# Optimization experiments

Measured on AMD Instinct MI355X. Metric: run time of the kernel, lower is better.

## Reference

```python
import jax, jax.numpy as jnp
import numpy as np

N_VERTICES = 2000
N_SENSORY = 784
N_EDGES = 500_000
BATCH = 32
T_STEPS = 5
LR_VALUES = 0.1


def setup_inputs() -> dict:
    key = jax.random.key(0)
    k1, k2, k3 = jax.random.split(key, 3)
    values = jax.random.normal(k1, (BATCH, N_VERTICES), dtype=jnp.float32)
    # weight_init 'normal 0.0' -> std = max(0.01, 0) = 0.01 in the torch module
    weights = jax.random.normal(k2, (N_EDGES,), dtype=jnp.float32) * 0.01
    edge_index = jax.random.randint(k3, (2, N_EDGES), 0, N_VERTICES, dtype=jnp.int32)
    # sensory nodes (first 784) are clamped; only internal nodes update
    update_mask = jnp.arange(N_VERTICES) >= N_SENSORY  # bool [N]
    return {
        "values": values,
        "weights": weights,
        "edge_index": edge_index,
        "update_mask": update_mask,
        "T": T_STEPS,
    }


def reference(values, weights, edge_index, update_mask, T):
    """Iterative predictive-coding message passing.

    Each step:
      pred_i  = sum_{e: dst(e)=i} w_e * f(values[src(e)])   (gather-mul-scatter)
      err     = values - pred
      back_j  = sum_{e: src(e)=j} w_e * err[dst(e)]          (reverse scatter)
      dv      = err - f'(values) * back                      (dE/dx)
      values  = values - lr * dv   (sensory nodes clamped)
    """
    src, dst = edge_index[0], edge_index[1]
    n = values.shape[1]
    mask = update_mask[None, :]

    def step(v, _):
        fx = jnp.tanh(v)                                   # [B, N]
        msg = weights[None, :] * fx[:, src]                # [B, E]
        pred = jax.ops.segment_sum(msg.T, dst, num_segments=n).T  # [B, N]
        err = v - pred                                     # [B, N]
        w_err = weights[None, :] * err[:, dst]             # [B, E]
        back = jax.ops.segment_sum(w_err.T, src, num_segments=n).T  # [B, N]
        fprime = 1.0 - fx * fx                             # tanh'
        dv = err - fprime * back
        v_new = jnp.where(mask, v - LR_VALUES * dv, v)
        return v_new, None

    v_final, _ = jax.lax.scan(step, values, None, length=T)
    return v_final
```

## Files before the change

### kernel.cpp

```cpp
#include <hip/hip_runtime.h>
#include <hip/hip_bf16.h>


#define N_V     2000
#define N_SENS  784
#define N_INT   (N_V - N_SENS)
#define N_E     500000
#define T_STEPS 5
#define LR_VAL  0.1f
#define NVB     (N_V * 32)
#define NVH     (N_V * 16)
#define KP      2016
#define NCH     63
#define NT1     125
#define NT2     76
#define FRAG_N  (2 * NCH * 64 * 8)
#define NBLK    250
#define EPB     2000

typedef float  f32x4 __attribute__((ext_vector_type(4)));
typedef short  s16x8 __attribute__((ext_vector_type(8)));

__device__ __forceinline__ float bits_to_f32(unsigned u) {
    union { unsigned u; float f; } c; c.u = u; return c.f;
}
__device__ __forceinline__ unsigned f32_to_bits(float f) {
    union { float f; unsigned u; } c; c.f = f; return c.u;
}
__device__ __forceinline__ unsigned short f32_to_bf16(float f) {
    unsigned u = f32_to_bits(f);
    return (unsigned short)((u + 0x7FFFu + ((u >> 16) & 1u)) >> 16);
}
__device__ __forceinline__ float bf16_to_f32(unsigned short s) {
    return bits_to_f32((unsigned)s << 16);
}

__device__ __forceinline__ int aposKB(int k, int b) {
    int c = k >> 5, q = (k >> 3) & 3, j = k & 7;
    int h = b >> 4, m = b & 15;
    return (((h * NCH + c) * 64) + q * 16 + m) * 8 + j;
}


__global__ __launch_bounds__(256) void k_cnt(const int* __restrict__ dst,
                                             int* __restrict__ cnt_g,
                                             unsigned short* __restrict__ fxA,
                                             unsigned short* __restrict__ errA) {
    __shared__ int cnt[NT1];
    int b = blockIdx.x;
    {
        int t = b * 256 + threadIdx.x;
        if (t < 16 * 32) {
            int k = 2000 + (t >> 5), bb = t & 31;
            fxA[aposKB(k, bb)] = 0;
            errA[aposKB(k, bb)] = 0;
        }
    }
    for (int i = threadIdx.x; i < NT1; i += 256) cnt[i] = 0;
    __syncthreads();
    int base = b * EPB;
    for (int e = base + threadIdx.x; e < base + EPB; e += 256)
        atomicAdd(&cnt[dst[e] >> 4], 1);
    __syncthreads();
    for (int t = threadIdx.x; t < NT1; t += 256)
        cnt_g[t * 256 + b] = cnt[t];
}

__global__ __launch_bounds__(256) void k_scan_a(const int* __restrict__ cnt_g,
                                                int* __restrict__ base_g,
                                                int* __restrict__ totals) {
    __shared__ int sh[256];
    int t = blockIdx.x, tid = threadIdx.x;
    int v = (tid < NBLK) ? cnt_g[t * 256 + tid] : 0;
    sh[tid] = v;
    __syncthreads();
    for (int off = 1; off < 256; off <<= 1) {
        int x = (tid >= off) ? sh[tid - off] : 0;
        __syncthreads();
        sh[tid] += x;
        __syncthreads();
    }
    if (tid < NBLK) base_g[t * 256 + tid] = sh[tid] - v;
    if (tid == 255) totals[t] = sh[255];
}

__global__ void k_scan_b(const int* __restrict__ totals, int* __restrict__ tile_start) {
    if (threadIdx.x == 0 && blockIdx.x == 0) {
        int acc = 0;
        for (int t = 0; t < NT1; ++t) { tile_start[t] = acc; acc += totals[t]; }
        tile_start[NT1] = acc;
    }
}

__global__ __launch_bounds__(256) void k_place(
        const int* __restrict__ src, const int* __restrict__ dst,
        const float* __restrict__ w, const int* __restrict__ base_g,
        const int* __restrict__ tile_start, unsigned* __restrict__ pk_g) {
    __shared__ int cur[NT1];
    int b = blockIdx.x;
    for (int t = threadIdx.x; t < NT1; t += 256)
        cur[t] = tile_start[t] + base_g[t * 256 + b];
    __syncthreads();
    int base = b * EPB;
    for (int e = base + threadIdx.x; e < base + EPB; e += 256) {
        int d = dst[e];
        unsigned pk = ((unsigned)f32_to_bf16(w[e]) << 16)
                    | ((unsigned)(d & 15) << 11) | (unsigned)src[e];
        int p = atomicAdd(&cur[d >> 4], 1);
        pk_g[p] = pk;
    }
}

__global__ __launch_bounds__(256) void k_build(
        const unsigned* __restrict__ pk_g, const int* __restrict__ tile_start,
        uint4* __restrict__ WAbf4, unsigned short* __restrict__ WAd) {
    __shared__ float acc[8][KP];
    int tile = blockIdx.x >> 1, half = blockIdx.x & 1;
    for (int i = threadIdx.x; i < 8 * KP / 4; i += 256)
        ((float4*)&acc[0][0])[i] = make_float4(0.f, 0.f, 0.f, 0.f);
    __syncthreads();
    int beg = tile_start[tile], end = tile_start[tile + 1];
    for (int e = beg + threadIdx.x; e < end; e += 256) {
        unsigned pk = pk_g[e];
        int row = (int)((pk >> 11) & 15u);
        if ((row >> 3) == half)
            atomicAdd(&acc[row & 7][pk & 0x7FFu], bf16_to_f32((unsigned short)(pk >> 16)));
    }
    __syncthreads();
    for (int i = threadIdx.x; i < 8 * 252; i += 256) {
        int rr = i / 252, g = i - rr * 252;
        int c = g >> 2, q = g & 3;
        int col = g * 8;
        unsigned short r[8];
        #pragma unroll
        for (int j = 0; j < 8; ++j) r[j] = f32_to_bf16(acc[rr][col + j]);
        uint4 val = *(const uint4*)r;
        int m = half * 8 + rr;
        WAbf4[((tile * NCH + c) * 64) + q * 16 + m] = val;
        *(uint4*)(WAd + (size_t)(tile * 16 + m) * KP + col) = val;
    }
}

__global__ void k_trB(const unsigned short* __restrict__ WAd, uint4* __restrict__ WBf4) {
    int t = blockIdx.x * blockDim.x + threadIdx.x;
    if (t < NT2 * NCH * 64) {
        int tile = t / (NCH * 64);
        int rem = t - tile * (NCH * 64);
        int c = rem >> 6, l = rem & 63;
        int jcol = N_SENS + tile * 16 + (l & 15);
        int k0 = c * 32 + (l >> 4) * 8;
        unsigned short r[8];
        #pragma unroll
        for (int j = 0; j < 8; ++j)
            r[j] = (k0 + j < N_V) ? WAd[(size_t)(k0 + j) * KP + jcol] : (unsigned short)0;
        WBf4[t] = *(const uint4*)r;
    }
}

__global__ void k_init(const float* __restrict__ vin, float* __restrict__ v,
                       unsigned short* __restrict__ fxA, float* __restrict__ out) {
    int t = blockIdx.x * blockDim.x + threadIdx.x;
    if (t < NVB) {
        float x = vin[t];
        int b = t / N_V;
        int i = t - b * N_V;
        v[(i << 5) + b] = x;
        fxA[aposKB(i, b)] = f32_to_bf16(tanhf(x));
        if (i < N_SENS) out[t] = x;
    }
}

__global__ __launch_bounds__(256) void k_gemm1(
        const uint4* __restrict__ WAbf4, const uint4* __restrict__ fxA4,
        const float* __restrict__ v_cur, unsigned short* __restrict__ errA) {
    __shared__ float red[1300];
    int bx = blockIdx.x, tid = threadIdx.x;
    int w = tid >> 6, l = tid & 63;
    int tile = bx >> 1, h = bx & 1;
    int cbeg = w * 16;
    const uint4* bp = WAbf4 + (size_t)tile * NCH * 64 + cbeg * 64 + l;
    const uint4* ap = fxA4 + (size_t)h * NCH * 64 + cbeg * 64 + l;
    f32x4 acc = {0.f, 0.f, 0.f, 0.f};
    #pragma unroll
    for (int cc = 0; cc < 16; ++cc) {
        if (cbeg + cc < NCH) {
            uint4 bfrag = bp[cc * 64];
            uint4 a = ap[cc * 64];
            acc = __builtin_amdgcn_mfma_f32_16x16x32_bf16(
                      *(s16x8*)&a, *(s16x8*)&bfrag, acc, 0, 0, 0);
        }
    }
    float* my = &red[w * 325 + l * 5];
    #pragma unroll
    for (int r = 0; r < 4; ++r) my[r] = acc[r];
    __syncthreads();
    if (w == 0) {
        float s[4];
        #pragma unroll
        for (int r = 0; r < 4; ++r)
            s[r] = red[l * 5 + r] + red[325 + l * 5 + r]
                 + red[650 + l * 5 + r] + red[975 + l * 5 + r];
        int i = tile * 16 + (l & 15);
        int q = l >> 4;
        int c2 = i >> 5, q2 = (i >> 3) & 3, j2 = i & 7;
        const float4 v4 = *(const float4*)(v_cur + (i << 5) + h * 16 + q * 4);
        int base = ((h * NCH + c2) * 64 + q2 * 16) * 8 + j2;
        errA[base + (q * 4 + 0) * 8] = f32_to_bf16(v4.x - s[0]);
        errA[base + (q * 4 + 1) * 8] = f32_to_bf16(v4.y - s[1]);
        errA[base + (q * 4 + 2) * 8] = f32_to_bf16(v4.z - s[2]);
        errA[base + (q * 4 + 3) * 8] = f32_to_bf16(v4.w - s[3]);
    }
}

__global__ __launch_bounds__(256) void k_gemm2(
        const uint4* __restrict__ WBf4, const uint4* __restrict__ errA4,
        unsigned short* __restrict__ errA, unsigned short* __restrict__ fxA,
        float* __restrict__ v_cur, float* __restrict__ out, int final_step) {
    __shared__ float red[1300];
    int bx = blockIdx.x, tid = threadIdx.x;
    int w = tid >> 6, l = tid & 63;
    int tile = bx >> 1, h = bx & 1;
    int cbeg = w * 16;
    const uint4* bp = WBf4 + (size_t)tile * NCH * 64 + cbeg * 64 + l;
    const uint4* ap = errA4 + (size_t)h * NCH * 64 + cbeg * 64 + l;
    f32x4 acc = {0.f, 0.f, 0.f, 0.f};
    #pragma unroll
    for (int cc = 0; cc < 16; ++cc) {
        if (cbeg + cc < NCH) {
            uint4 bfrag = bp[cc * 64];
            uint4 a = ap[cc * 64];
            acc = __builtin_amdgcn_mfma_f32_16x16x32_bf16(
                      *(s16x8*)&a, *(s16x8*)&bfrag, acc, 0, 0, 0);
        }
    }
    float* my = &red[w * 325 + l * 5];
    #pragma unroll
    for (int r = 0; r < 4; ++r) my[r] = acc[r];
    __syncthreads();
    if (w == 0) {
        float s[4];
        #pragma unroll
        for (int r = 0; r < 4; ++r)
            s[r] = red[l * 5 + r] + red[325 + l * 5 + r]
                 + red[650 + l * 5 + r] + red[975 + l * 5 + r];
        int j = N_SENS + tile * 16 + (l & 15);
        int q = l >> 4;
        int c2 = j >> 5, q2 = (j >> 3) & 3, j2 = j & 7;
        float4 v4 = *(const float4*)(v_cur + (j << 5) + h * 16 + q * 4);
        int base = ((h * NCH + c2) * 64 + q2 * 16) * 8 + j2;
        float vv[4] = {v4.x, v4.y, v4.z, v4.w};
        #pragma unroll
        for (int r = 0; r < 4; ++r) {
            float e0 = bf16_to_f32(errA[base + (q * 4 + r) * 8]);
            float fxv = tanhf(vv[r]);
            float vn = vv[r] - LR_VAL * (e0 - (1.f - fxv * fxv) * s[r]);
            vv[r] = vn;
            fxA[base + (q * 4 + r) * 8] = f32_to_bf16(tanhf(vn));
        }
        float4 o = {vv[0], vv[1], vv[2], vv[3]};
        *(float4*)(v_cur + (j << 5) + h * 16 + q * 4) = o;
        if (final_step) {
            #pragma unroll
            for (int r = 0; r < 4; ++r) {
                int b = h * 16 + q * 4 + r;
                out[b * N_V + j] = vv[r];
            }
        }
    }
}


__global__ void k_zero_i32(int* a, int n) {
    int t = blockIdx.x * blockDim.x + threadIdx.x;
    if (t < n) a[t] = 0;
}

__global__ void k_hist(const int* __restrict__ src, const int* __restrict__ dst,
                       int* cnt_dst, int* cnt_src) {
    int e = blockIdx.x * blockDim.x + threadIdx.x;
    if (e < N_E) {
        atomicAdd(&cnt_dst[dst[e]], 1);
        atomicAdd(&cnt_src[src[e]], 1);
    }
}

__global__ __launch_bounds__(1024) void k_scan(int* cnt_a, int* rp_a,
                                               int* cnt_b, int* rp_b) {
    __shared__ int sh[1024];
    int t = threadIdx.x;
    for (int pass = 0; pass < 2; ++pass) {
        int* cnt = pass ? cnt_b : cnt_a;
        int* rp  = pass ? rp_b  : rp_a;
        int i0 = 2 * t, i1 = 2 * t + 1;
        int c0 = (i0 < N_V) ? cnt[i0] : 0;
        int c1 = (i1 < N_V) ? cnt[i1] : 0;
        __syncthreads();
        sh[t] = c0 + c1;
        __syncthreads();
        for (int off = 1; off < 1024; off <<= 1) {
            int v = (t >= off) ? sh[t - off] : 0;
            __syncthreads();
            sh[t] += v;
            __syncthreads();
        }
        int incl = sh[t];
        int e0 = incl - (c0 + c1);
        int e1 = e0 + c0;
        if (i0 <= N_V) rp[i0] = e0;
        if (i1 <= N_V) rp[i1] = e1;
        if (i0 < N_V) cnt[i0] = e0;
        if (i1 < N_V) cnt[i1] = e1;
    }
}

__global__ void k_scatter(const int* __restrict__ src, const int* __restrict__ dst,
                          const float* __restrict__ w,
                          int* cur_dst, int* cur_src,
                          unsigned* __restrict__ pk_dst, unsigned* __restrict__ pk_src) {
    int e = blockIdx.x * blockDim.x + threadIdx.x;
    if (e < N_E) {
        int s = src[e], d = dst[e];
        unsigned wbits = (unsigned)f32_to_bf16(w[e]);
        int p = atomicAdd(&cur_dst[d], 1);
        pk_dst[p] = (wbits << 16) | (unsigned)s;
        int q = atomicAdd(&cur_src[s], 1);
        pk_src[q] = (wbits << 16) | (unsigned)d;
    }
}

__global__ void k_cast_in(const float* __restrict__ vin, float* __restrict__ v) {
    int t = blockIdx.x * blockDim.x + threadIdx.x;
    if (t < NVB) {
        int i = t >> 5, b = t & 31;
        v[t] = vin[b * N_V + i];
    }
}

__global__ void k_fx_csr(const float* __restrict__ v, unsigned short* __restrict__ fx) {
    int t = blockIdx.x * blockDim.x + threadIdx.x;
    if (t < NVB) {
        int i = t >> 5, b = t & 31;
        int h = b >> 4, b16 = b & 15;
        fx[h * NVH + i * 16 + b16] = f32_to_bf16(tanhf(v[t]));
    }
}

__global__ __launch_bounds__(256) void k_pred_err(
        const float* __restrict__ v, const unsigned short* __restrict__ fx,
        const int* __restrict__ rp, const unsigned* __restrict__ pk,
        unsigned short* __restrict__ err) {
    __shared__ unsigned short tab[NVH];
    int h  = blockIdx.x / 250;
    int vg = blockIdx.x % 250;
    {
        const uint4* g = (const uint4*)(fx + h * NVH);
        uint4* l = (uint4*)tab;
        for (int i = threadIdx.x; i < NVH / 8; i += 256) l[i] = g[i];
    }
    __syncthreads();
    int wave = threadIdx.x >> 6;
    int lane = threadIdx.x & 63;
    int b16 = lane & 15, epar = lane >> 4;
    for (int k = 0; k < 2; ++k) {
        int vid = vg * 8 + wave * 2 + k;
        int beg = rp[vid], end = rp[vid + 1];
        float sum = 0.f;
        for (int e = beg + epar; e < end; e += 4) {
            unsigned p = pk[e];
            float w = bits_to_f32(p & 0xFFFF0000u);
            int nb = (int)(p & 0xFFFFu);
            sum += w * bf16_to_f32(tab[nb * 16 + b16]);
        }
        sum += __shfl_xor(sum, 16, 64);
        sum += __shfl_xor(sum, 32, 64);
        if (epar == 0) {
            float vo = v[(vid << 5) + h * 16 + b16];
            err[h * NVH + vid * 16 + b16] = f32_to_bf16(vo - sum);
        }
    }
}

__global__ __launch_bounds__(256) void k_back_upd(
        const unsigned short* __restrict__ fx, const unsigned short* __restrict__ err,
        const int* __restrict__ rp, const unsigned* __restrict__ pk,
        float* __restrict__ v) {
    __shared__ unsigned short tab[NVH];
    int h  = blockIdx.x / 152;
    int vg = blockIdx.x % 152;
    {
        const uint4* g = (const uint4*)(err + h * NVH);
        uint4* l = (uint4*)tab;
        for (int i = threadIdx.x; i < NVH / 8; i += 256) l[i] = g[i];
    }
    __syncthreads();
    int wave = threadIdx.x >> 6;
    int lane = threadIdx.x & 63;
    int b16 = lane & 15, epar = lane >> 4;
    for (int k = 0; k < 2; ++k) {
        int vid = N_SENS + vg * 8 + wave * 2 + k;
        if (vid >= N_V) continue;
        int beg = rp[vid], end = rp[vid + 1];
        float sum = 0.f;
        for (int e = beg + epar; e < end; e += 4) {
            unsigned p = pk[e];
            float w = bits_to_f32(p & 0xFFFF0000u);
            int nb = (int)(p & 0xFFFFu);
            sum += w * bf16_to_f32(tab[nb * 16 + b16]);
        }
        sum += __shfl_xor(sum, 16, 64);
        sum += __shfl_xor(sum, 32, 64);
        if (epar == 0) {
            float e0  = bf16_to_f32(tab[vid * 16 + b16]);
            float fxv = bf16_to_f32(fx[h * NVH + vid * 16 + b16]);
            float dv = e0 - (1.f - fxv * fxv) * sum;
            v[(vid << 5) + h * 16 + b16] -= LR_VAL * dv;
        }
    }
}

__global__ void k_out_fb(const float* __restrict__ v, float* __restrict__ out) {
    int t = blockIdx.x * blockDim.x + threadIdx.x;
    if (t < NVB) {
        int b = t / N_V;
        int i = t - b * N_V;
        out[t] = v[(i << 5) + b];
    }
}


extern "C" void kernel_launch(void* const* d_in, const int* in_sizes, int n_in,
                              void* d_out, int out_size, void* d_ws, size_t ws_size,
                              hipStream_t stream) {
    const float* vals = (const float*)d_in[0];
    const float* wts  = (const float*)d_in[1];
    const int* ei = (const int*)d_in[2];
    const int* src = ei;
    const int* dst = ei + N_E;
    float* out = (float*)d_out;

    const int EB = (N_E + 255) / 256;

    const size_t WABF_T = (size_t)NT1 * NCH * 64;
    const size_t WBF_T  = (size_t)NT2 * NCH * 64;
    const size_t WAD_N  = (size_t)N_V * KP;
    const size_t need = (size_t)N_E * 4 + 2 * NT1 * 256 * 4 + 512 * 4
                      + WAD_N * 2 + WABF_T * 16 + WBF_T * 16
                      + 2 * (size_t)FRAG_N * 2 + NVB * 4 + 256;

    if (ws_size >= need) {
        unsigned* pk_g = (unsigned*)d_ws;
        int* cnt_g  = (int*)(pk_g + N_E);
        int* base_g = cnt_g + NT1 * 256;
        int* totals = base_g + NT1 * 256;
        int* tile_start = totals + 128;
        unsigned short* WAd = (unsigned short*)(tile_start + 384);
        uint4* WAbf4 = (uint4*)(WAd + WAD_N);
        uint4* WBf4  = WAbf4 + WABF_T;
        unsigned short* fxA  = (unsigned short*)(WBf4 + WBF_T);
        unsigned short* errA = fxA + FRAG_N;
        float* v_cur = (float*)(errA + FRAG_N);

        k_cnt<<<NBLK, 256, 0, stream>>>(dst, cnt_g, fxA, errA);
        k_scan_a<<<NT1, 256, 0, stream>>>(cnt_g, base_g, totals);
        k_scan_b<<<1, 64, 0, stream>>>(totals, tile_start);
        k_place<<<NBLK, 256, 0, stream>>>(src, dst, wts, base_g, tile_start, pk_g);
        k_build<<<2 * NT1, 256, 0, stream>>>(pk_g, tile_start, WAbf4, WAd);
        k_trB<<<(int)((WBF_T + 255) / 256), 256, 0, stream>>>(WAd, WBf4);
        k_init<<<250, 256, 0, stream>>>(vals, v_cur, fxA, out);

        for (int t = 0; t < T_STEPS; ++t) {
            k_gemm1<<<250, 256, 0, stream>>>(WAbf4, (const uint4*)fxA, v_cur, errA);
            k_gemm2<<<152, 256, 0, stream>>>(WBf4, (const uint4*)errA, errA, fxA,
                                             v_cur, out, (t == T_STEPS - 1) ? 1 : 0);
        }
    } else {
        float* v_cur = (float*)d_ws;
        unsigned short* fx_g  = (unsigned short*)(v_cur + NVB);
        unsigned short* err_g = fx_g + NVB;
        int* rp_dst  = (int*)(err_g + NVB);
        int* rp_src  = rp_dst + 2048;
        int* cur_dst = rp_src + 2048;
        int* cur_src = cur_dst + 2048;
        unsigned* pk_dst = (unsigned*)(cur_src + 2048);
        unsigned* pk_src = pk_dst + N_E;

        k_zero_i32<<<16, 256, 0, stream>>>(cur_dst, 4096);
        k_hist<<<EB, 256, 0, stream>>>(src, dst, cur_dst, cur_src);
        k_scan<<<1, 1024, 0, stream>>>(cur_dst, rp_dst, cur_src, rp_src);
        k_scatter<<<EB, 256, 0, stream>>>(src, dst, wts, cur_dst, cur_src,
                                          pk_dst, pk_src);
        k_cast_in<<<250, 256, 0, stream>>>(vals, v_cur);
        for (int t = 0; t < T_STEPS; ++t) {
            k_fx_csr<<<250, 256, 0, stream>>>(v_cur, fx_g);
            k_pred_err<<<500, 256, 0, stream>>>(v_cur, fx_g, rp_dst, pk_dst, err_g);
            k_back_upd<<<304, 256, 0, stream>>>(fx_g, err_g, rp_src, pk_src, v_cur);
        }
        k_out_fb<<<250, 256, 0, stream>>>(v_cur, out);
    }
}
```

Baseline: 172.0 us.

## Use one wave per tile covering both batch halves, drop LDS split-K reduction

Each GEMM block becomes a single 64-thread wave that walks the full K dimension and computes both batch halves, reusing each loaded weight fragment for two MFMAs. This removes the 4-wave split-K, the shared-memory reduction and the __syncthreads, and halves weight-fragment loads from global memory. In exchange the grid shrinks to 125 and 76 single-wave blocks, so far fewer waves are resident on the GPU and each wave runs a serial chain of 63 dependent MFMAs per accumulator, which may leave latency exposed.

```diff
diff --git a/kernel.cpp b/kernel.cpp
--- a/kernel.cpp
+++ b/kernel.cpp
@@ -170,82 +170,66 @@
     }
 }
 
-__global__ __launch_bounds__(256) void k_gemm1(
+__global__ __launch_bounds__(64) void k_gemm1(
         const uint4* __restrict__ WAbf4, const uint4* __restrict__ fxA4,
         const float* __restrict__ v_cur, unsigned short* __restrict__ errA) {
-    __shared__ float red[1300];
-    int bx = blockIdx.x, tid = threadIdx.x;
-    int w = tid >> 6, l = tid & 63;
-    int tile = bx >> 1, h = bx & 1;
-    int cbeg = w * 16;
-    const uint4* bp = WAbf4 + (size_t)tile * NCH * 64 + cbeg * 64 + l;
-    const uint4* ap = fxA4 + (size_t)h * NCH * 64 + cbeg * 64 + l;
-    f32x4 acc = {0.f, 0.f, 0.f, 0.f};
+    int tile = blockIdx.x;
+    int l = threadIdx.x;
+    const uint4* bp  = WAbf4 + (size_t)tile * NCH * 64 + l;
+    const uint4* a0p = fxA4 + l;
+    const uint4* a1p = fxA4 + (size_t)NCH * 64 + l;
+    f32x4 acc0 = {0.f, 0.f, 0.f, 0.f}, acc1 = {0.f, 0.f, 0.f, 0.f};
+    #pragma unroll 7
+    for (int c = 0; c < NCH; ++c) {
+        uint4 bfrag = bp[c * 64];
+        uint4 a0 = a0p[c * 64];
+        uint4 a1 = a1p[c * 64];
+        acc0 = __builtin_amdgcn_mfma_f32_16x16x32_bf16(
+                   *(s16x8*)&a0, *(s16x8*)&bfrag, acc0, 0, 0, 0);
+        acc1 = __builtin_amdgcn_mfma_f32_16x16x32_bf16(
+                   *(s16x8*)&a1, *(s16x8*)&bfrag, acc1, 0, 0, 0);
+    }
+    int i = tile * 16 + (l & 15);
+    int q = l >> 4;
+    int c2 = i >> 5, q2 = (i >> 3) & 3, j2 = i & 7;
     #pragma unroll
-    for (int cc = 0; cc < 16; ++cc) {
-        if (cbeg + cc < NCH) {
-            uint4 bfrag = bp[cc * 64];
-            uint4 a = ap[cc * 64];
-            acc = __builtin_amdgcn_mfma_f32_16x16x32_bf16(
-                      *(s16x8*)&a, *(s16x8*)&bfrag, acc, 0, 0, 0);
-        }
-    }
-    float* my = &red[w * 325 + l * 5];
-    #pragma unroll
-    for (int r = 0; r < 4; ++r) my[r] = acc[r];
-    __syncthreads();
-    if (w == 0) {
-        float s[4];
-        #pragma unroll
-        for (int r = 0; r < 4; ++r)
-            s[r] = red[l * 5 + r] + red[325 + l * 5 + r]
-                 + red[650 + l * 5 + r] + red[975 + l * 5 + r];
-        int i = tile * 16 + (l & 15);
-        int q = l >> 4;
-        int c2 = i >> 5, q2 = (i >> 3) & 3, j2 = i & 7;
+    for (int h = 0; h < 2; ++h) {
+        f32x4 acc = h ? acc1 : acc0;
         const float4 v4 = *(const float4*)(v_cur + (i << 5) + h * 16 + q * 4);
         int base = ((h * NCH + c2) * 64 + q2 * 16) * 8 + j2;
-        errA[base + (q * 4 + 0) * 8] = f32_to_bf16(v4.x - s[0]);
-        errA[base + (q * 4 + 1) * 8] = f32_to_bf16(v4.y - s[1]);
-        errA[base + (q * 4 + 2) * 8] = f32_to_bf16(v4.z - s[2]);
-        errA[base + (q * 4 + 3) * 8] = f32_to_bf16(v4.w - s[3]);
-    }
-}
-
-__global__ __launch_bounds__(256) void k_gemm2(
+        errA[base + (q * 4 + 0) * 8] = f32_to_bf16(v4.x - acc[0]);
+        errA[base + (q * 4 + 1) * 8] = f32_to_bf16(v4.y - acc[1]);
+        errA[base + (q * 4 + 2) * 8] = f32_to_bf16(v4.z - acc[2]);
+        errA[base + (q * 4 + 3) * 8] = f32_to_bf16(v4.w - acc[3]);
+    }
+}
+
+__global__ __launch_bounds__(64) void k_gemm2(
         const uint4* __restrict__ WBf4, const uint4* __restrict__ errA4,
         unsigned short* __restrict__ errA, unsigned short* __restrict__ fxA,
         float* __restrict__ v_cur, float* __restrict__ out, int final_step) {
-    __shared__ float red[1300];
-    int bx = blockIdx.x, tid = threadIdx.x;
-    int w = tid >> 6, l = tid & 63;
-    int tile = bx >> 1, h = bx & 1;
-    int cbeg = w * 16;
-    const uint4* bp = WBf4 + (size_t)tile * NCH * 64 + cbeg * 64 + l;
-    const uint4* ap = errA4 + (size_t)h * NCH * 64 + cbeg * 64 + l;
-    f32x4 acc = {0.f, 0.f, 0.f, 0.f};
+    int tile = blockIdx.x;
+    int l = threadIdx.x;
+    const uint4* bp  = WBf4 + (size_t)tile * NCH * 64 + l;
+    const uint4* a0p = errA4 + l;
+    const uint4* a1p = errA4 + (size_t)NCH * 64 + l;
+    f32x4 acc0 = {0.f, 0.f, 0.f, 0.f}, acc1 = {0.f, 0.f, 0.f, 0.f};
+    #pragma unroll 7
+    for (int c = 0; c < NCH; ++c) {
+        uint4 bfrag = bp[c * 64];
+        uint4 a0 = a0p[c * 64];
+        uint4 a1 = a1p[c * 64];
+        acc0 = __builtin_amdgcn_mfma_f32_16x16x32_bf16(
+                   *(s16x8*)&a0, *(s16x8*)&bfrag, acc0, 0, 0, 0);
+        acc1 = __builtin_amdgcn_mfma_f32_16x16x32_bf16(
+                   *(s16x8*)&a1, *(s16x8*)&bfrag, acc1, 0, 0, 0);
+    }
+    int j = N_SENS + tile * 16 + (l & 15);
+    int q = l >> 4;
+    int c2 = j >> 5, q2 = (j >> 3) & 3, j2 = j & 7;
     #pragma unroll
-    for (int cc = 0; cc < 16; ++cc) {
-        if (cbeg + cc < NCH) {
-            uint4 bfrag = bp[cc * 64];
-            uint4 a = ap[cc * 64];
-            acc = __builtin_amdgcn_mfma_f32_16x16x32_bf16(
-                      *(s16x8*)&a, *(s16x8*)&bfrag, acc, 0, 0, 0);
-        }
-    }
-    float* my = &red[w * 325 + l * 5];
-    #pragma unroll
-    for (int r = 0; r < 4; ++r) my[r] = acc[r];
-    __syncthreads();
-    if (w == 0) {
-        float s[4];
-        #pragma unroll
-        for (int r = 0; r < 4; ++r)
-            s[r] = red[l * 5 + r] + red[325 + l * 5 + r]
-                 + red[650 + l * 5 + r] + red[975 + l * 5 + r];
-        int j = N_SENS + tile * 16 + (l & 15);
-        int q = l >> 4;
-        int c2 = j >> 5, q2 = (j >> 3) & 3, j2 = j & 7;
+    for (int h = 0; h < 2; ++h) {
+        f32x4 acc = h ? acc1 : acc0;
         float4 v4 = *(const float4*)(v_cur + (j << 5) + h * 16 + q * 4);
         int base = ((h * NCH + c2) * 64 + q2 * 16) * 8 + j2;
         float vv[4] = {v4.x, v4.y, v4.z, v4.w};
@@ -253,7 +237,7 @@
         for (int r = 0; r < 4; ++r) {
             float e0 = bf16_to_f32(errA[base + (q * 4 + r) * 8]);
             float fxv = tanhf(vv[r]);
-            float vn = vv[r] - LR_VAL * (e0 - (1.f - fxv * fxv) * s[r]);
+            float vn = vv[r] - LR_VAL * (e0 - (1.f - fxv * fxv) * acc[r]);
             vv[r] = vn;
             fxA[base + (q * 4 + r) * 8] = f32_to_bf16(tanhf(vn));
         }
@@ -469,9 +453,9 @@
         k_init<<<250, 256, 0, stream>>>(vals, v_cur, fxA, out);
 
         for (int t = 0; t < T_STEPS; ++t) {
-            k_gemm1<<<250, 256, 0, stream>>>(WAbf4, (const uint4*)fxA, v_cur, errA);
-            k_gemm2<<<152, 256, 0, stream>>>(WBf4, (const uint4*)errA, errA, fxA,
-                                             v_cur, out, (t == T_STEPS - 1) ? 1 : 0);
+            k_gemm1<<<NT1, 64, 0, stream>>>(WAbf4, (const uint4*)fxA, v_cur, errA);
+            k_gemm2<<<NT2, 64, 0, stream>>>(WBf4, (const uint4*)errA, errA, fxA,
+                                            v_cur, out, (t == T_STEPS - 1) ? 1 : 0);
         }
     } else {
         float* v_cur = (float*)d_ws;
```

Result: slower. 221.4 us (+28.7%).
